# Performance work log

Measured on AMD Instinct MI355X. Metric: run time of the kernel, lower is better.

Reference implementation:

```python
import jax, jax.numpy as jnp
import numpy as np

REACH = 2
BS = 32  # blocksize
NHID = 15  # nlayers - 1
CI = 12    # 2*(reach+1)*reach


def _offsets():
    # matches get_nb ordering: rows above (dy=-2,-1; dx=-2..2), then left (dy=0; dx=-2,-1)
    offs = [(dy, dx) for dy in range(-REACH, 0) for dx in range(-REACH, REACH + 1)]
    offs += [(0, dx) for dx in range(-REACH, 0)]
    return offs


def setup_inputs() -> dict:
    key = jax.random.key(0)
    k0, k1, k2, k3, k4 = jax.random.split(key, 5)
    x = jax.random.uniform(k0, (8, 3, 512, 512), jnp.float32, -1.0, 1.0)
    s = 1.0 / np.sqrt(CI).astype(np.float32)
    Wh = jax.random.uniform(k1, (NHID, CI, CI), jnp.float32, -s, s)
    bh = jax.random.uniform(k2, (NHID, CI), jnp.float32, -s, s)
    Wo = jax.random.uniform(k3, (1, CI), jnp.float32, -s, s)
    bo = jax.random.uniform(k4, (1,), jnp.float32, -s, s)
    return {"x": x, "Wh": Wh, "bh": bh, "Wo": Wo, "bo": bo}


def reference(x, Wh, bh, Wo, bo):
    b, c, h, w = x.shape
    h = h // BS * BS
    w = w // BS * BS
    x = x[:, :, :h, :w]
    nbh, nbw = h // BS, w // BS
    # unfold into (nbc, BS, BS) blocks, matching torch unfold/unfold/reshape
    blocks = x.reshape(b, c, nbh, BS, nbw, BS).transpose(0, 1, 2, 4, 3, 5).reshape(-1, BS, BS)
    xp = jnp.pad(blocks, ((0, 0), (REACH, REACH), (REACH, REACH)))
    # batched causal-neighbor gather: (nbc, BS, BS, 12)
    feats = jnp.stack(
        [xp[:, REACH + dy:REACH + dy + BS, REACH + dx:REACH + dx + BS] for dy, dx in _offsets()],
        axis=-1,
    )
    hdn = feats
    for l in range(NHID):
        hdn = jax.nn.leaky_relu(jnp.einsum('nhwi,oi->nhwo', hdn, Wh[l]) + bh[l])
    pred = jnp.clip(jnp.einsum('nhwi,oi->nhwo', hdn, Wo)[..., 0] + bo[0], -1.0, 1.0)
    deltas = jnp.fmod(blocks - pred + 1.0, 2.0) - 1.0
    deltas = deltas.reshape(b * c, h * w)
    loss1 = 255.0 * jnp.sqrt(jnp.mean(jnp.square(deltas)))
    return (loss1, deltas)
```

## Files before the change

kernel.cpp:

```cpp
#include <hip/hip_runtime.h>
#include <math.h>

#define CI 12
#define NHID 15
#define NBLK 6144
#define NPIX (NBLK * 1024)

typedef int   i32x2 __attribute__((ext_vector_type(2)));
typedef float f32x2 __attribute__((ext_vector_type(2)));

static __device__ __forceinline__ int h2pack(float lo, float hi) {
    auto h = __builtin_amdgcn_cvt_pkrtz(lo, hi);
    int r;
    __builtin_memcpy(&r, &h, 4);
    return r;
}

#define LKA \
  "v_cvt_pkrtz_f16_f32 v36, v44, v45\n" \
  "v_cvt_pkrtz_f16_f32 v37, v46, v47\n" \
  "v_pk_mul_f16 v60, s21, v36\n" \
  "v_pk_mul_f16 v61, s21, v37\n" \
  "v_pk_max_f16 v36, v36, v60\n" \
  "v_pk_max_f16 v37, v37, v61\n"
#define LKB \
  "v_cvt_pkrtz_f16_f32 v38, v48, v49\n" \
  "v_cvt_pkrtz_f16_f32 v39, v50, v51\n" \
  "v_pk_mul_f16 v60, s21, v38\n" \
  "v_pk_mul_f16 v61, s21, v39\n" \
  "v_pk_max_f16 v38, v38, v60\n" \
  "v_pk_max_f16 v39, v39, v61\n"
#define LKC \
  "v_cvt_pkrtz_f16_f32 v40, v52, v53\n" \
  "v_cvt_pkrtz_f16_f32 v41, v54, v55\n" \
  "v_pk_mul_f16 v60, s21, v40\n" \
  "v_pk_mul_f16 v61, s21, v41\n" \
  "v_pk_max_f16 v40, v40, v60\n" \
  "v_pk_max_f16 v41, v41, v61\n"
#define LKD \
  "v_cvt_pkrtz_f16_f32 v42, v56, v57\n" \
  "v_cvt_pkrtz_f16_f32 v43, v58, v59\n" \
  "v_pk_mul_f16 v60, s21, v42\n" \
  "v_pk_mul_f16 v61, s21, v43\n" \
  "v_pk_max_f16 v42, v42, v60\n" \
  "v_pk_max_f16 v43, v43, v61\n"

#define MFA(w) "v_mfma_f32_16x16x16_f16 v[44:47], %[" w "], v[36:37], v[32:35]\n"
#define MFB(w) "v_mfma_f32_16x16x16_f16 v[48:51], %[" w "], v[38:39], v[32:35]\n"
#define MFC(w) "v_mfma_f32_16x16x16_f16 v[52:55], %[" w "], v[40:41], v[32:35]\n"
#define MFD(w) "v_mfma_f32_16x16x16_f16 v[56:59], %[" w "], v[42:43], v[32:35]\n"

#define LAYER(w) LKA LKB MFA(w) LKC MFB(w) LKD MFC(w) "s_nop 1\n" MFD(w)

#define DSLOADS(EN) do {                                                      \
    const unsigned aA = ldsbase + (unsigned)(((EN) + offA) * 4);              \
    const unsigned aB = ldsbase + (unsigned)(((EN) + offB) * 4);              \
    const unsigned aV = ldsbase + (unsigned)((EN) * 4);                       \
    asm volatile("ds_read2_b32 %0, %1 offset0:0 offset1:1"   : "=v"(a01) : "v"(aA)); \
    asm volatile("ds_read2_b32 %0, %1 offset0:16 offset1:17" : "=v"(a23) : "v"(aA)); \
    asm volatile("ds_read2_b32 %0, %1 offset0:37 offset1:38" : "=v"(a45) : "v"(aA)); \
    asm volatile("ds_read2_b32 %0, %1 offset0:53 offset1:54" : "=v"(a67) : "v"(aA)); \
    asm volatile("ds_read2_b32 %0, %1 offset0:0 offset1:37"  : "=v"(b02) : "v"(aB)); \
    asm volatile("ds_read2_b32 %0, %1 offset0:16 offset1:53" : "=v"(b13) : "v"(aB)); \
    asm volatile("ds_read2_b32 %0, %1 offset0:74 offset1:90" : "=v"(b45) : "v"(aB)); \
    asm volatile("ds_read2_b32 %0, %1 offset0:0 offset1:16"  : "=v"(v01) : "v"(aV)); \
    asm volatile("ds_read2_b32 %0, %1 offset0:37 offset1:53" : "=v"(v23) : "v"(aV)); \
} while (0)

#define DSWAIT() asm volatile("s_waitcnt lgkmcnt(0)"                          \
    : "+v"(a01), "+v"(a23), "+v"(a45), "+v"(a67),                             \
      "+v"(b02), "+v"(b13), "+v"(b45), "+v"(v01), "+v"(v23))

#define PACKF() do {                                                          \
    fa0 = q3 ? 0x3C00 : h2pack(a01.x, a01.y);                                 \
    fb0 = q3 ? 0x3C00 : h2pack(a23.x, a23.y);                                 \
    fc0 = q3 ? 0x3C00 : h2pack(a45.x, a45.y);                                 \
    fd0 = q3 ? 0x3C00 : h2pack(a67.x, a67.y);                                 \
    fa1 = q3 ? 0 : h2pack(b02.x, b02.y);                                      \
    fb1 = q3 ? 0 : h2pack(b13.x, b13.y);                                      \
    fc1 = q3 ? 0 : h2pack(b02.y, b45.x);                                      \
    fd1 = q3 ? 0 : h2pack(b13.y, b45.y);                                      \
    vA = v01.x; vB = v01.y; vC = v23.x; vD = v23.y;                           \
} while (0)

__global__ __launch_bounds__(256, 4) void codec_main(
    const float* __restrict__ x,
    const float* __restrict__ Wh,
    const float* __restrict__ bh,
    const float* __restrict__ Wo,
    const float* __restrict__ bo,
    float* __restrict__ out,
    float* __restrict__ loss_acc)
{
    __shared__ float tile[36 * 37];
    __shared__ float stage[4][256];
    __shared__ float wsum[4];

    const int n    = blockIdx.x;
    const int tid  = threadIdx.x;
    const int lane = tid & 63;
    const int wv   = tid >> 6;
    const int t    = lane & 15;
    const int q    = lane >> 4;

    {
        const int col = tid & 31;
        const int r0  = tid >> 5;
        #pragma unroll
        for (int i = 0; i < 6; ++i) {
            int idx = tid + i * 256;
            if (idx < 36 * 37) tile[idx] = 0.0f;
        }
        __syncthreads();
        const int bc  = n >> 8;
        const int blk = n & 255;
        const int by  = blk >> 4;
        const int bx  = blk & 15;
        #pragma unroll
        for (int p = 0; p < 4; ++p) {
            const int row = r0 + 8 * p;
            tile[(row + 2) * 37 + col + 2] =
                x[((size_t)bc * 512 + (size_t)(by * 32 + row)) * 512
                  + (size_t)(bx * 32 + col)];
        }
        __syncthreads();
    }

    const int kA = (q == 0) ? 3 : (q == 1) ? 8 : 10;
    i32x2 wq[16];
    #pragma unroll
    for (int l = 0; l < NHID; ++l) {
        int w0 = 0, w1 = 0;
        if (q < 3 && t < CI) {
            const float* wr = Wh + l * (CI * CI) + t * CI;
            w0 = h2pack(wr[kA], wr[kA + 1]);
            w1 = h2pack(wr[q],  wr[q + 5]);
        }
        if (q == 3 && t < CI)  w0 = h2pack(bh[l * CI + t], 0.f);
        if (q == 3 && t == CI) w0 = 0x3C00;
        wq[l] = (i32x2){ w0, w1 };
    }
    {
        int w0 = 0, w1 = 0;
        if (t == 0 && q < 3) {
            w0 = h2pack(Wo[kA], Wo[kA + 1]);
            w1 = h2pack(Wo[q],  Wo[q + 5]);
        }
        if (t == 0 && q == 3) w0 = h2pack(bo[0], 0.f);
        wq[15] = (i32x2){ w0, w1 };
    }

    const int sh8  = q * 8;
    const int offA = (int)(signed char)((0x00FEDCB7u >> sh8) & 0xFFu);
    const int offB = (int)(signed char)((0x00B6B5B4u >> sh8) & 0xFFu);
    const bool q3  = (q == 3);
    const unsigned ldsbase = (unsigned)(uintptr_t)(&tile[0]);

    int e = (wv * 8 + 2) * 37 + (t + 2);

    f32x2 a01, a23, a45, a67, b02, b13, b45, v01, v23;
    int fa0, fa1, fb0, fb1, fc0, fc1, fd0, fd1;
    float vA, vB, vC, vD;

    DSLOADS(e);
    DSWAIT();
    PACKF();

    float d2 = 0.0f;
    #pragma unroll 1
    for (int yi = 0; yi < 4; ++yi) {
        const int en = (yi < 3) ? e + 74 : e;
        DSLOADS(en);

        float pA, pB, pC, pD;
        asm volatile(
            "s_mov_b32 s21, 0x211f211f\n"
            "v_mov_b32 v32, 0\n" "v_mov_b32 v33, 0\n"
            "v_mov_b32 v34, 0\n" "v_mov_b32 v35, 0\n"
            "v_mov_b32 v36, %[fa0]\n" "v_mov_b32 v37, %[fa1]\n"
            "v_mov_b32 v38, %[fb0]\n" "v_mov_b32 v39, %[fb1]\n"
            "v_mov_b32 v40, %[fc0]\n" "v_mov_b32 v41, %[fc1]\n"
            "v_mov_b32 v42, %[fd0]\n" "v_mov_b32 v43, %[fd1]\n"
            MFA("w0") MFB("w0") MFC("w0") MFD("w0")
            "s_nop 7\n" "s_nop 7\n" "s_nop 7\n" "s_nop 4\n"
            LAYER("w1")  LAYER("w2")  LAYER("w3")  LAYER("w4")
            LAYER("w5")  LAYER("w6")  LAYER("w7")  LAYER("w8")
            LAYER("w9")  LAYER("w10") LAYER("w11") LAYER("w12")
            LAYER("w13") LAYER("w14") LAYER("w15")
            "v_mov_b32 %[pA], v44\n"
            "s_nop 1\n"
            "v_mov_b32 %[pB], v48\n"
            "s_nop 7\n" "s_nop 7\n"
            "v_mov_b32 %[pC], v52\n"
            "s_nop 3\n"
            "v_mov_b32 %[pD], v56\n"
            : [pA] "=v"(pA), [pB] "=v"(pB), [pC] "=v"(pC), [pD] "=v"(pD)
            : [w0] "a"(wq[0]),  [w1] "a"(wq[1]),  [w2] "a"(wq[2]),
              [w3] "a"(wq[3]),  [w4] "a"(wq[4]),  [w5] "a"(wq[5]),
              [w6] "a"(wq[6]),  [w7] "a"(wq[7]),  [w8] "a"(wq[8]),
              [w9] "a"(wq[9]),  [w10] "a"(wq[10]), [w11] "a"(wq[11]),
              [w12] "a"(wq[12]), [w13] "a"(wq[13]), [w14] "a"(wq[14]),
              [w15] "a"(wq[15]),
              [fa0] "v"(fa0), [fa1] "v"(fa1), [fb0] "v"(fb0), [fb1] "v"(fb1),
              [fc0] "v"(fc0), [fc1] "v"(fc1), [fd0] "v"(fd0), [fd1] "v"(fd1)
            : "s21",
              "v32","v33","v34","v35","v36","v37","v38","v39",
              "v40","v41","v42","v43","v44","v45","v46","v47",
              "v48","v49","v50","v51","v52","v53","v54","v55",
              "v56","v57","v58","v59","v60","v61");

        DSWAIT();

        if (lane < 16) {
            const float qA = fminf(fmaxf(pA, -1.0f), 1.0f);
            const float uA = vA - qA + 1.0f;
            const float dA = uA - ((uA < 2.0f) ? 1.0f : 3.0f);
            const float qB = fminf(fmaxf(pB, -1.0f), 1.0f);
            const float uB = vB - qB + 1.0f;
            const float dB = uB - ((uB < 2.0f) ? 1.0f : 3.0f);
            const float qC = fminf(fmaxf(pC, -1.0f), 1.0f);
            const float uC = vC - qC + 1.0f;
            const float dC = uC - ((uC < 2.0f) ? 1.0f : 3.0f);
            const float qD = fminf(fmaxf(pD, -1.0f), 1.0f);
            const float uD = vD - qD + 1.0f;
            const float dD = uD - ((uD < 2.0f) ? 1.0f : 3.0f);
            const int r = 2 * yi;
            stage[wv][r * 32 + t]            = dA;
            stage[wv][r * 32 + 16 + t]       = dB;
            stage[wv][(r + 1) * 32 + t]      = dC;
            stage[wv][(r + 1) * 32 + 16 + t] = dD;
            d2 = fmaf(dA, dA, fmaf(dB, dB, fmaf(dC, dC, fmaf(dD, dD, d2))));
        }
        e = en;
        PACKF();
    }

    float* outp = out + 1 + (size_t)n * 1024 + wv * 256;
    #pragma unroll
    for (int j = 0; j < 4; ++j)
        outp[j * 64 + lane] = stage[wv][j * 64 + lane];

    #pragma unroll
    for (int off = 8; off > 0; off >>= 1) d2 += __shfl_down(d2, off, 64);
    if (lane == 0) wsum[wv] = d2;
    __syncthreads();
    if (tid == 0) atomicAdd(loss_acc, wsum[0] + wsum[1] + wsum[2] + wsum[3]);
}

__global__ void codec_loss(const float* __restrict__ acc, float* __restrict__ out)
{
    out[0] = 255.0f * sqrtf(acc[0] / (float)NPIX);
}

extern "C" void kernel_launch(void* const* d_in, const int* in_sizes, int n_in,
                              void* d_out, int out_size, void* d_ws, size_t ws_size,
                              hipStream_t stream)
{
    const float* x  = (const float*)d_in[0];
    const float* Wh = (const float*)d_in[1];
    const float* bh = (const float*)d_in[2];
    const float* Wo = (const float*)d_in[3];
    const float* bo = (const float*)d_in[4];
    float* out = (float*)d_out;
    float* acc = (float*)d_ws;

    hipMemsetAsync(acc, 0, sizeof(float), stream);
    codec_main<<<NBLK, 256, 0, stream>>>(x, Wh, bh, Wo, bo, out, acc);
    codec_loss<<<1, 1, 0, stream>>>(acc, out);
}
```

Before: 192.2 us.

## Write deltas directly to global, fuse final loss, raise occupancy bound

Drops the shared-memory stage buffer and stores each wave's delta values straight to global memory inside the loop. The separate one-thread loss kernel is replaced by a last-block-done counter that computes the final loss inside the main kernel. The leaky-relu temporaries reuse accumulator registers, which frees two VGPRs, and the launch bound goes from 4 to 5 blocks per SIMD. In exchange, the direct stores are narrower 16-lane writes per row, and the extra atomic counter adds a little per-block work.

```diff
diff --git a/kernel.cpp b/kernel.cpp
--- a/kernel.cpp
+++ b/kernel.cpp
@@ -19,31 +19,31 @@
 #define LKA \
   "v_cvt_pkrtz_f16_f32 v36, v44, v45\n" \
   "v_cvt_pkrtz_f16_f32 v37, v46, v47\n" \
-  "v_pk_mul_f16 v60, s21, v36\n" \
-  "v_pk_mul_f16 v61, s21, v37\n" \
-  "v_pk_max_f16 v36, v36, v60\n" \
-  "v_pk_max_f16 v37, v37, v61\n"
+  "v_pk_mul_f16 v44, s21, v36\n" \
+  "v_pk_mul_f16 v45, s21, v37\n" \
+  "v_pk_max_f16 v36, v36, v44\n" \
+  "v_pk_max_f16 v37, v37, v45\n"
 #define LKB \
   "v_cvt_pkrtz_f16_f32 v38, v48, v49\n" \
   "v_cvt_pkrtz_f16_f32 v39, v50, v51\n" \
-  "v_pk_mul_f16 v60, s21, v38\n" \
-  "v_pk_mul_f16 v61, s21, v39\n" \
-  "v_pk_max_f16 v38, v38, v60\n" \
-  "v_pk_max_f16 v39, v39, v61\n"
+  "v_pk_mul_f16 v48, s21, v38\n" \
+  "v_pk_mul_f16 v49, s21, v39\n" \
+  "v_pk_max_f16 v38, v38, v48\n" \
+  "v_pk_max_f16 v39, v39, v49\n"
 #define LKC \
   "v_cvt_pkrtz_f16_f32 v40, v52, v53\n" \
   "v_cvt_pkrtz_f16_f32 v41, v54, v55\n" \
-  "v_pk_mul_f16 v60, s21, v40\n" \
-  "v_pk_mul_f16 v61, s21, v41\n" \
-  "v_pk_max_f16 v40, v40, v60\n" \
-  "v_pk_max_f16 v41, v41, v61\n"
+  "v_pk_mul_f16 v52, s21, v40\n" \
+  "v_pk_mul_f16 v53, s21, v41\n" \
+  "v_pk_max_f16 v40, v40, v52\n" \
+  "v_pk_max_f16 v41, v41, v53\n"
 #define LKD \
   "v_cvt_pkrtz_f16_f32 v42, v56, v57\n" \
   "v_cvt_pkrtz_f16_f32 v43, v58, v59\n" \
-  "v_pk_mul_f16 v60, s21, v42\n" \
-  "v_pk_mul_f16 v61, s21, v43\n" \
-  "v_pk_max_f16 v42, v42, v60\n" \
-  "v_pk_max_f16 v43, v43, v61\n"
+  "v_pk_mul_f16 v56, s21, v42\n" \
+  "v_pk_mul_f16 v57, s21, v43\n" \
+  "v_pk_max_f16 v42, v42, v56\n" \
+  "v_pk_max_f16 v43, v43, v57\n"
 
 #define MFA(w) "v_mfma_f32_16x16x16_f16 v[44:47], %[" w "], v[36:37], v[32:35]\n"
 #define MFB(w) "v_mfma_f32_16x16x16_f16 v[48:51], %[" w "], v[38:39], v[32:35]\n"
@@ -83,7 +83,7 @@
     vA = v01.x; vB = v01.y; vC = v23.x; vD = v23.y;                           \
 } while (0)
 
-__global__ __launch_bounds__(256, 4) void codec_main(
+__global__ __launch_bounds__(256, 5) void codec_main(
     const float* __restrict__ x,
     const float* __restrict__ Wh,
     const float* __restrict__ bh,
@@ -93,7 +93,6 @@
     float* __restrict__ loss_acc)
 {
     __shared__ float tile[36 * 37];
-    __shared__ float stage[4][256];
     __shared__ float wsum[4];
 
     const int n    = blockIdx.x;
@@ -157,6 +156,7 @@
     const unsigned ldsbase = (unsigned)(uintptr_t)(&tile[0]);
 
     int e = (wv * 8 + 2) * 37 + (t + 2);
+    float* ob = out + 1 + (size_t)n * 1024 + wv * 256 + t;
 
     f32x2 a01, a23, a45, a67, b02, b13, b45, v01, v23;
     int fa0, fa1, fb0, fb1, fc0, fc1, fd0, fd1;
@@ -207,7 +207,7 @@
               "v32","v33","v34","v35","v36","v37","v38","v39",
               "v40","v41","v42","v43","v44","v45","v46","v47",
               "v48","v49","v50","v51","v52","v53","v54","v55",
-              "v56","v57","v58","v59","v60","v61");
+              "v56","v57","v58","v59");
 
         DSWAIT();
 
@@ -224,32 +224,31 @@
             const float qD = fminf(fmaxf(pD, -1.0f), 1.0f);
             const float uD = vD - qD + 1.0f;
             const float dD = uD - ((uD < 2.0f) ? 1.0f : 3.0f);
-            const int r = 2 * yi;
-            stage[wv][r * 32 + t]            = dA;
-            stage[wv][r * 32 + 16 + t]       = dB;
-            stage[wv][(r + 1) * 32 + t]      = dC;
-            stage[wv][(r + 1) * 32 + 16 + t] = dD;
+            float* op = ob + yi * 64;
+            op[0]  = dA;
+            op[16] = dB;
+            op[32] = dC;
+            op[48] = dD;
             d2 = fmaf(dA, dA, fmaf(dB, dB, fmaf(dC, dC, fmaf(dD, dD, d2))));
         }
         e = en;
         PACKF();
     }
-
-    float* outp = out + 1 + (size_t)n * 1024 + wv * 256;
-    #pragma unroll
-    for (int j = 0; j < 4; ++j)
-        outp[j * 64 + lane] = stage[wv][j * 64 + lane];
 
     #pragma unroll
     for (int off = 8; off > 0; off >>= 1) d2 += __shfl_down(d2, off, 64);
     if (lane == 0) wsum[wv] = d2;
     __syncthreads();
-    if (tid == 0) atomicAdd(loss_acc, wsum[0] + wsum[1] + wsum[2] + wsum[3]);
-}
-
-__global__ void codec_loss(const float* __restrict__ acc, float* __restrict__ out)
-{
-    out[0] = 255.0f * sqrtf(acc[0] / (float)NPIX);
+    if (tid == 0) {
+        atomicAdd(loss_acc, wsum[0] + wsum[1] + wsum[2] + wsum[3]);
+        __threadfence();
+        unsigned old = atomicAdd((unsigned*)(loss_acc + 1), 1u);
+        if (old == (unsigned)(NBLK - 1)) {
+            __threadfence();
+            float a = atomicAdd(loss_acc, 0.0f);
+            out[0] = 255.0f * sqrtf(a / (float)NPIX);
+        }
+    }
 }
 
 extern "C" void kernel_launch(void* const* d_in, const int* in_sizes, int n_in,
@@ -264,7 +263,6 @@
     float* out = (float*)d_out;
     float* acc = (float*)d_ws;
 
-    hipMemsetAsync(acc, 0, sizeof(float), stream);
+    hipMemsetAsync(acc, 0, 2 * sizeof(float), stream);
     codec_main<<<NBLK, 256, 0, stream>>>(x, Wh, bh, Wo, bo, out, acc);
-    codec_loss<<<1, 1, 0, stream>>>(acc, out);
 }
```

New measurement: 345.9 us. 1.8x slower.
